# Optimization experiments

Hardware: AMD Instinct MI355X
Metric: run time of the kernel (lower is better)

Reference implementation:

```python
import jax, jax.numpy as jnp
import numpy as np

B, CIN, COUT, K, H, W = 16, 128, 256, 3, 56, 56
STRIDE = 1
PAD = K // 2


def setup_inputs() -> dict:
    key = jax.random.key(0)
    ks = jax.random.split(key, 12)
    x = jax.random.normal(ks[0], (B, CIN, H, W), dtype=jnp.float32)
    base_kernel = jax.random.normal(ks[1], (COUT, CIN, K, K), dtype=jnp.float32)
    bias = jnp.zeros((COUT,), dtype=jnp.float32)
    s = 1.0 / np.sqrt(CIN)
    fc_spatial_w = jax.random.uniform(ks[2], (K * K, CIN), minval=-s, maxval=s)
    fc_spatial_b = jax.random.uniform(ks[3], (K * K,), minval=-s, maxval=s)
    fc_in_w = jax.random.uniform(ks[4], (CIN, CIN), minval=-s, maxval=s)
    fc_in_b = jax.random.uniform(ks[5], (CIN,), minval=-s, maxval=s)
    fc_out_w = jax.random.uniform(ks[6], (COUT, CIN), minval=-s, maxval=s)
    fc_out_b = jax.random.uniform(ks[7], (COUT,), minval=-s, maxval=s)
    fc_kernel_w = jax.random.uniform(ks[8], (COUT * CIN * K * K, CIN), minval=-s, maxval=s)
    fc_kernel_b = jax.random.uniform(ks[9], (COUT * CIN * K * K,), minval=-s, maxval=s)
    return {
        "x": x, "base_kernel": base_kernel, "bias": bias,
        "fc_spatial_w": fc_spatial_w, "fc_spatial_b": fc_spatial_b,
        "fc_in_w": fc_in_w, "fc_in_b": fc_in_b,
        "fc_out_w": fc_out_w, "fc_out_b": fc_out_b,
        "fc_kernel_w": fc_kernel_w, "fc_kernel_b": fc_kernel_b,
    }


def _odconv(x, base_kernel, bias, fc_spatial_w, fc_spatial_b, fc_in_w, fc_in_b,
            fc_out_w, fc_out_b, fc_kernel_w, fc_kernel_b):
    b = x.shape[0]
    # global average pool -> context [B, Cin]
    context = jnp.mean(x, axis=(2, 3))
    sig = jax.nn.sigmoid
    attn_spatial = sig(context @ fc_spatial_w.T + fc_spatial_b).reshape(b, 1, 1, K, K)
    attn_in = sig(context @ fc_in_w.T + fc_in_b).reshape(b, 1, CIN, 1, 1)
    attn_out = sig(context @ fc_out_w.T + fc_out_b).reshape(b, COUT, 1, 1, 1)
    attn_kernel = sig(context @ fc_kernel_w.T + fc_kernel_b).reshape(b, COUT, CIN, K, K)
    # 5-way broadcast multiply -> per-sample dynamic kernel [B, Cout, Cin, K, K]
    dyn = base_kernel[None] * attn_out * attn_in * attn_spatial * attn_kernel

    def conv_one(xi, wi):
        # xi: [Cin, H, W], wi: [Cout, Cin, K, K]
        out = jax.lax.conv_general_dilated(
            xi[None], wi,
            window_strides=(STRIDE, STRIDE),
            padding=[(PAD, PAD), (PAD, PAD)],
            dimension_numbers=("NCHW", "OIHW", "NCHW"),
        )
        return out[0]

    out = jax.vmap(conv_one)(x, dyn)  # [B, Cout, H', W']
    return out + bias[None, :, None, None]


def reference(x, base_kernel, bias, fc_spatial_w, fc_spatial_b, fc_in_w, fc_in_b,
              fc_out_w, fc_out_b, fc_kernel_w, fc_kernel_b):
    return _odconv(x, base_kernel, bias, fc_spatial_w, fc_spatial_b, fc_in_w, fc_in_b,
                   fc_out_w, fc_out_b, fc_kernel_w, fc_kernel_b)
```

## Files before the change

kernel.cpp:

```cpp
#include <hip/hip_runtime.h>
#include <hip/hip_bf16.h>
#include <math.h>

#define BATCH 16
#define CIN   128
#define COUT  256
#define HH    56
#define WW    56
#define HW    3136
#define NTAP  9
#define NE    (COUT*CIN*NTAP)

typedef short short8 __attribute__((ext_vector_type(8)));
typedef float floatx4 __attribute__((ext_vector_type(4)));

#define WSB_CTX   0
#define WSB_ASP   8192
#define WSB_AIN   9472
#define WSB_AOUT  17664
#define WSB_ZP    34048
#define WSB_XT    38144
#define WSB_DYN   (WSB_XT + BATCH*HW*CIN*2)

static __device__ inline unsigned short f2b(float f) {
    union { float f; unsigned u; } v; v.f = f;
    unsigned r = v.u + 0x7FFF + ((v.u >> 16) & 1);
    return (unsigned short)(r >> 16);
}
static __device__ inline short8 pack8(float4 a, float4 b) {
    short8 r;
    r[0] = (short)f2b(a.x); r[1] = (short)f2b(a.y); r[2] = (short)f2b(a.z); r[3] = (short)f2b(a.w);
    r[4] = (short)f2b(b.x); r[5] = (short)f2b(b.y); r[6] = (short)f2b(b.z); r[7] = (short)f2b(b.w);
    return r;
}

typedef const __attribute__((address_space(1))) void* gas_ptr;
typedef __attribute__((address_space(3))) void* las_ptr;
static __device__ __forceinline__ void gl_lds16(const void* g, void* l) {
    __builtin_amdgcn_global_load_lds((gas_ptr)g, (las_ptr)l, 16, 0, 0);
}

__global__ void k_context(const float* __restrict__ x, float* __restrict__ ctx,
                          float* __restrict__ zp) {
    int bc = blockIdx.x;
    if (bc == 0 && threadIdx.x < 64) {
        uint4 z = {0u, 0u, 0u, 0u};
        ((uint4*)zp)[threadIdx.x] = z;
    }
    const float4* p = (const float4*)(x + (size_t)bc * HW);
    float s = 0.f;
    for (int i = threadIdx.x; i < HW / 4; i += 256) { float4 v = p[i]; s += v.x + v.y + v.z + v.w; }
    for (int off = 32; off; off >>= 1) s += __shfl_down(s, off, 64);
    __shared__ float red[4];
    if ((threadIdx.x & 63) == 0) red[threadIdx.x >> 6] = s;
    __syncthreads();
    if (threadIdx.x == 0) ctx[bc] = (red[0] + red[1] + red[2] + red[3]) * (1.f / (float)HW);
}

__global__ void k_attn(const float* __restrict__ ctx,
                       const float* __restrict__ wsp, const float* __restrict__ bsp,
                       const float* __restrict__ win, const float* __restrict__ bin,
                       const float* __restrict__ wout, const float* __restrict__ bout,
                       float* __restrict__ asp, float* __restrict__ ain, float* __restrict__ aout) {
    int R = blockIdx.x * 4 + (threadIdx.x >> 6);
    int lane = threadIdx.x & 63;
    int b = R / 393, r = R % 393;
    const float* w; float bias; float* o;
    if (r < 9)        { w = wsp  + r * CIN;         bias = bsp[r];         o = asp  + b * 16  + r; }
    else if (r < 137) { w = win  + (r - 9) * CIN;   bias = bin[r - 9];     o = ain  + b * CIN + (r - 9); }
    else              { w = wout + (r - 137) * CIN; bias = bout[r - 137];  o = aout + b * COUT + (r - 137); }
    float2 wv = ((const float2*)w)[lane];
    float2 cv = ((const float2*)(ctx + b * CIN))[lane];
    float d = wv.x * cv.x + wv.y * cv.y;
    for (int off = 32; off; off >>= 1) d += __shfl_down(d, off, 64);
    if (lane == 0) *o = 1.f / (1.f + __expf(-(d + bias)));
}

#define XT_BLOCKS    784
#define BUILD_BLOCKS 1152
__global__ void k_fat(const float* __restrict__ x, unsigned short* __restrict__ xt,
                      const float* __restrict__ ctx, const float* __restrict__ wk,
                      const float* __restrict__ bk, const float* __restrict__ base,
                      const float* __restrict__ asp, const float* __restrict__ ain,
                      const float* __restrict__ aout, unsigned short* __restrict__ dyn) {
    __shared__ unsigned short s_res[9 * 530 + 16];
    if (blockIdx.x < XT_BLOCKS) {
        int bid = blockIdx.x;
        int b = bid / 49;
        int p = (bid % 49) * 64 + (threadIdx.x & 63);
        int icq = threadIdx.x >> 6;
        const float* xb = x + (size_t)b * CIN * HW + p;
        unsigned short tmp[32];
#pragma unroll
        for (int j = 0; j < 32; ++j) tmp[j] = f2b(xb[(size_t)(icq * 32 + j) * HW]);
        uint4* dst = (uint4*)(xt + ((size_t)b * HW + p) * CIN + icq * 32);
        const uint4* s = (const uint4*)tmp;
        dst[0] = s[0]; dst[1] = s[1]; dst[2] = s[2]; dst[3] = s[3];
        return;
    }
    int bid = blockIdx.x - XT_BLOCKS;
    int wid = threadIdx.x >> 6, l = threadIdx.x & 63;
    int lq = l & 15, quad = l >> 4;
    int e0      = bid * 256;
    int siteMin = e0 / 9;

    short8 afr[4];
    const float* arow = ctx + lq * CIN;
#pragma unroll
    for (int kc = 0; kc < 4; ++kc) {
        float4 v0 = *(const float4*)(arow + kc * 32 + quad * 8);
        float4 v1 = *(const float4*)(arow + kc * 32 + quad * 8 + 4);
        afr[kc] = pack8(v0, v1);
    }

    int ebase = e0 + wid * 64;
    short8 bfr[4][4];
    float bke[4], bse[4];
#pragma unroll
    for (int j = 0; j < 4; ++j) {
        unsigned e = ebase + j * 16 + lq;
        const float* wrow = wk + (size_t)e * CIN;
#pragma unroll
        for (int kc = 0; kc < 4; ++kc) {
            float4 v0 = *(const float4*)(wrow + kc * 32 + quad * 8);
            float4 v1 = *(const float4*)(wrow + kc * 32 + quad * 8 + 4);
            bfr[j][kc] = pack8(v0, v1);
        }
        bke[j] = bk[e]; bse[j] = base[e];
    }
    floatx4 acc[4];
#pragma unroll
    for (int j = 0; j < 4; ++j) acc[j] = (floatx4){0.f, 0.f, 0.f, 0.f};
#pragma unroll
    for (int j = 0; j < 4; ++j)
#pragma unroll
        for (int kc = 0; kc < 4; ++kc)
            acc[j] = __builtin_amdgcn_mfma_f32_16x16x32_bf16(afr[kc], bfr[j][kc], acc[j], 0, 0, 0);
#pragma unroll
    for (int j = 0; j < 4; ++j) {
        unsigned e = ebase + j * 16 + lq;
        unsigned site = e / 9u, tap = e - site * 9u;
        unsigned oc = site >> 7, ic = site & 127;
        unsigned ds = site - siteMin;
#pragma unroll
        for (int r = 0; r < 4; ++r) {
            int b = quad * 4 + r;
            float s = 1.f / (1.f + __expf(-(acc[j][r] + bke[j])));
            float v = bse[j] * s * aout[b * COUT + oc] * ain[b * CIN + ic] * asp[b * 16 + tap];
            s_res[tap * 530 + b * 32 + ds] = f2b(v);
        }
    }
    __syncthreads();
    int hw_id = threadIdx.x >> 5;
    int hl    = threadIdx.x & 31;
#pragma unroll
    for (int it = 0; it < 18; ++it) {
        int pair = it * 8 + hw_id;
        int t = pair >> 4, b = pair & 15;
        int sLo = (e0 - t + 8) / 9;
        int sHi = (e0 + 255 - t) / 9;
        int cnt = sHi - sLo + 1;
        if (hl < cnt) {
            unsigned short v = s_res[t * 530 + b * 32 + (sLo - siteMin) + hl];
            dyn[(size_t)b * NE + t * 32768 + sLo + hl] = v;
        }
    }
}

__global__ __launch_bounds__(256, 2) void k_conv(
    const unsigned short* __restrict__ xt, const unsigned short* __restrict__ dyn,
    const float* __restrict__ bias, float* __restrict__ out,
    const unsigned short* __restrict__ zp) {
    __shared__ char s_x[640 * 64];
    __shared__ char s_a[576 * 64];
    int id  = blockIdx.x;
    int low = id & 7;
    int q   = id >> 3;
    int r   = q % 7;
    int phi = q / 7;
    int p   = phi * 8 + low;
    int oc0 = (p >> 4) * 64;
    int b   = p & 15;
    int r0  = r * 8;

    int tid = threadIdx.x;
    int wn = tid >> 6, l = tid & 63, lq = l & 15, quad = l >> 4;
    const unsigned short* xtb  = xt  + (size_t)b * HW * CIN;
    const unsigned short* dynb = dyn + (size_t)b * NE;

    int colx = wn * 16 + (l >> 2);
    int gxs  = colx - 1;
    bool gxok = (unsigned)gxs < (unsigned)WW;
    const unsigned short* zsrc = zp + l * 8;

    int pixaddr[7];
#pragma unroll
    for (int nf = 0; nf < 7; ++nf) {
        int n = nf * 16 + lq;
        int tr = wn * 2 + n / 56, col = n % 56;
        pixaddr[nf] = (tr * 64 + col) * 64 + quad * 16;
    }

    floatx4 acc[4][7];
#pragma unroll
    for (int i = 0; i < 4; ++i)
#pragma unroll
        for (int j = 0; j < 7; ++j) acc[i][j] = (floatx4){0.f, 0.f, 0.f, 0.f};

    for (int kc = 0; kc < 4; ++kc) {
        __syncthreads();
#pragma unroll
        for (int ry = 0; ry < 10; ++ry) {
            int gy = r0 + ry - 1;
            const unsigned short* src =
                (gxok && (unsigned)gy < (unsigned)HH)
                    ? xtb + (size_t)(gy * WW + gxs) * CIN + kc * 32 + (l & 3) * 8
                    : zsrc;
            gl_lds16(src, s_x + ry * 4096 + wn * 1024);
        }
#pragma unroll
        for (int i = 0; i < 9; ++i) {
            int u = i * 256 + tid;
            int icq2 = u & 3, oc = (u >> 2) & 63, tap = u >> 8;
            gl_lds16(dynb + (size_t)(tap * COUT + oc0 + oc) * CIN + kc * 32 + icq2 * 8,
                     s_a + i * 4096 + wn * 1024);
        }
        __syncthreads();
        __builtin_amdgcn_s_setprio(1);
#pragma unroll
        for (int tap = 0; tap < 9; ++tap) {
            short8 af[4];
#pragma unroll
            for (int mf = 0; mf < 4; ++mf)
                af[mf] = *(const short8*)(s_a + (tap * 64 + mf * 16 + lq) * 64 + quad * 16);
            int toff = (tap / 3) * 4096 + (tap % 3) * 64;
#pragma unroll
            for (int nf = 0; nf < 7; ++nf) {
                short8 bf = *(const short8*)(s_x + pixaddr[nf] + toff);
#pragma unroll
                for (int mf = 0; mf < 4; ++mf)
                    acc[mf][nf] = __builtin_amdgcn_mfma_f32_16x16x32_bf16(af[mf], bf, acc[mf][nf], 0, 0, 0);
            }
        }
        __builtin_amdgcn_s_setprio(0);
    }

#pragma unroll
    for (int mf = 0; mf < 4; ++mf) {
#pragma unroll
        for (int rr = 0; rr < 4; ++rr) {
            int oc = oc0 + mf * 16 + quad * 4 + rr;
            float bs = bias[oc];
            float* ob = out + (size_t)(b * COUT + oc) * HW + (r0 + wn * 2) * 56 + lq;
#pragma unroll
            for (int nf = 0; nf < 7; ++nf)
                ob[nf * 16] = acc[mf][nf][rr] + bs;
        }
    }
}

extern "C" void kernel_launch(void* const* d_in, const int* in_sizes, int n_in,
                              void* d_out, int out_size, void* d_ws, size_t ws_size,
                              hipStream_t stream) {
    const float* x    = (const float*)d_in[0];
    const float* base = (const float*)d_in[1];
    const float* bias = (const float*)d_in[2];
    const float* wsp  = (const float*)d_in[3];
    const float* bsp  = (const float*)d_in[4];
    const float* win  = (const float*)d_in[5];
    const float* bin  = (const float*)d_in[6];
    const float* wout = (const float*)d_in[7];
    const float* bout = (const float*)d_in[8];
    const float* wk   = (const float*)d_in[9];
    const float* bk   = (const float*)d_in[10];
    float* out = (float*)d_out;
    char* ws = (char*)d_ws;

    float* ctx  = (float*)(ws + WSB_CTX);
    float* asp  = (float*)(ws + WSB_ASP);
    float* ain  = (float*)(ws + WSB_AIN);
    float* aout = (float*)(ws + WSB_AOUT);
    float* zp   = (float*)(ws + WSB_ZP);
    unsigned short* xt  = (unsigned short*)(ws + WSB_XT);
    unsigned short* dyn = (unsigned short*)(ws + WSB_DYN);

    k_context<<<BATCH * CIN, 256, 0, stream>>>(x, ctx, zp);
    k_attn<<<(BATCH * 393) / 4, 256, 0, stream>>>(ctx, wsp, bsp, win, bin, wout, bout, asp, ain, aout);
    k_fat<<<XT_BLOCKS + BUILD_BLOCKS, 256, 0, stream>>>(x, xt, ctx, wk, bk, base, asp, ain, aout, dyn);
    k_conv<<<448, 256, 0, stream>>>(xt, dyn, bias, out, (const unsigned short*)zp);
}
```

Before: 313.9 us.

## Split fused transpose/build kernel; LDS-staged vectorized x transpose and register-pressure-reduced build

Splits the combined kernel into a dedicated x-transpose kernel and a dynamic-weight build kernel. The transpose now loads float4 along pixels into shared memory and writes 32-channel bf16 rows, replacing strided scalar loads. The build kernel processes its four column groups in two halves under launch_bounds(256,4) to cut register pressure and raise occupancy. It adds one kernel launch and loses any overlap between the transpose and build work inside a single grid.

```diff
diff --git a/kernel.cpp b/kernel.cpp
--- a/kernel.cpp
+++ b/kernel.cpp
@@ -76,29 +76,48 @@
     if (lane == 0) *o = 1.f / (1.f + __expf(-(d + bias)));
 }
 
-#define XT_BLOCKS    784
+#define XT_V2_BLOCKS (BATCH * 4 * 13)
+__global__ __launch_bounds__(256) void k_xt(const float* __restrict__ x,
+                                            unsigned short* __restrict__ xt) {
+    __shared__ unsigned short s[32 * 264];
+    int bid = blockIdx.x;
+    int b = bid / 52, rem = bid % 52;
+    int chg = rem / 13, ck = rem % 13;
+    int px0 = ck * 256;
+    int npx = HW - px0; if (npx > 256) npx = 256;
+    int tid = threadIdx.x;
+    const float* xb = x + ((size_t)(b * CIN + chg * 32)) * HW + px0;
+#pragma unroll
+    for (int pass = 0; pass < 8; ++pass) {
+        int i = pass * 256 + tid;
+        int c = i >> 6, p4 = i & 63;
+        int px = p4 * 4;
+        if (px < npx) {
+            float4 v = *(const float4*)(xb + (size_t)c * HW + px);
+            unsigned short h[4] = {f2b(v.x), f2b(v.y), f2b(v.z), f2b(v.w)};
+            *(uint2*)(&s[c * 264 + px]) = *(const uint2*)h;
+        }
+    }
+    __syncthreads();
+    int px = tid;
+    if (px < npx) {
+        unsigned short h[32];
+#pragma unroll
+        for (int c = 0; c < 32; ++c) h[c] = s[c * 264 + px];
+        uint4* dst = (uint4*)(xt + ((size_t)b * HW + px0 + px) * CIN + chg * 32);
+        const uint4* q = (const uint4*)h;
+        dst[0] = q[0]; dst[1] = q[1]; dst[2] = q[2]; dst[3] = q[3];
+    }
+}
+
 #define BUILD_BLOCKS 1152
-__global__ void k_fat(const float* __restrict__ x, unsigned short* __restrict__ xt,
-                      const float* __restrict__ ctx, const float* __restrict__ wk,
-                      const float* __restrict__ bk, const float* __restrict__ base,
-                      const float* __restrict__ asp, const float* __restrict__ ain,
-                      const float* __restrict__ aout, unsigned short* __restrict__ dyn) {
+__global__ __launch_bounds__(256, 4) void k_build(
+    const float* __restrict__ ctx, const float* __restrict__ wk,
+    const float* __restrict__ bk, const float* __restrict__ base,
+    const float* __restrict__ asp, const float* __restrict__ ain,
+    const float* __restrict__ aout, unsigned short* __restrict__ dyn) {
     __shared__ unsigned short s_res[9 * 530 + 16];
-    if (blockIdx.x < XT_BLOCKS) {
-        int bid = blockIdx.x;
-        int b = bid / 49;
-        int p = (bid % 49) * 64 + (threadIdx.x & 63);
-        int icq = threadIdx.x >> 6;
-        const float* xb = x + (size_t)b * CIN * HW + p;
-        unsigned short tmp[32];
-#pragma unroll
-        for (int j = 0; j < 32; ++j) tmp[j] = f2b(xb[(size_t)(icq * 32 + j) * HW]);
-        uint4* dst = (uint4*)(xt + ((size_t)b * HW + p) * CIN + icq * 32);
-        const uint4* s = (const uint4*)tmp;
-        dst[0] = s[0]; dst[1] = s[1]; dst[2] = s[2]; dst[3] = s[3];
-        return;
-    }
-    int bid = blockIdx.x - XT_BLOCKS;
+    int bid = blockIdx.x;
     int wid = threadIdx.x >> 6, l = threadIdx.x & 63;
     int lq = l & 15, quad = l >> 4;
     int e0      = bid * 256;
@@ -114,40 +133,44 @@
     }
 
     int ebase = e0 + wid * 64;
-    short8 bfr[4][4];
-    float bke[4], bse[4];
-#pragma unroll
-    for (int j = 0; j < 4; ++j) {
-        unsigned e = ebase + j * 16 + lq;
-        const float* wrow = wk + (size_t)e * CIN;
-#pragma unroll
-        for (int kc = 0; kc < 4; ++kc) {
-            float4 v0 = *(const float4*)(wrow + kc * 32 + quad * 8);
-            float4 v1 = *(const float4*)(wrow + kc * 32 + quad * 8 + 4);
-            bfr[j][kc] = pack8(v0, v1);
-        }
-        bke[j] = bk[e]; bse[j] = base[e];
-    }
-    floatx4 acc[4];
-#pragma unroll
-    for (int j = 0; j < 4; ++j) acc[j] = (floatx4){0.f, 0.f, 0.f, 0.f};
-#pragma unroll
-    for (int j = 0; j < 4; ++j)
-#pragma unroll
-        for (int kc = 0; kc < 4; ++kc)
-            acc[j] = __builtin_amdgcn_mfma_f32_16x16x32_bf16(afr[kc], bfr[j][kc], acc[j], 0, 0, 0);
-#pragma unroll
-    for (int j = 0; j < 4; ++j) {
-        unsigned e = ebase + j * 16 + lq;
-        unsigned site = e / 9u, tap = e - site * 9u;
-        unsigned oc = site >> 7, ic = site & 127;
-        unsigned ds = site - siteMin;
-#pragma unroll
-        for (int r = 0; r < 4; ++r) {
-            int b = quad * 4 + r;
-            float s = 1.f / (1.f + __expf(-(acc[j][r] + bke[j])));
-            float v = bse[j] * s * aout[b * COUT + oc] * ain[b * CIN + ic] * asp[b * 16 + tap];
-            s_res[tap * 530 + b * 32 + ds] = f2b(v);
+#pragma unroll
+    for (int jp = 0; jp < 2; ++jp) {
+        short8 bfr[2][4];
+        float bke[2], bse[2];
+        floatx4 acc[2];
+#pragma unroll
+        for (int u = 0; u < 2; ++u) {
+            int j = jp * 2 + u;
+            unsigned e = ebase + j * 16 + lq;
+            const float* wrow = wk + (size_t)e * CIN;
+#pragma unroll
+            for (int kc = 0; kc < 4; ++kc) {
+                float4 v0 = *(const float4*)(wrow + kc * 32 + quad * 8);
+                float4 v1 = *(const float4*)(wrow + kc * 32 + quad * 8 + 4);
+                bfr[u][kc] = pack8(v0, v1);
+            }
+            bke[u] = bk[e]; bse[u] = base[e];
+            acc[u] = (floatx4){0.f, 0.f, 0.f, 0.f};
+        }
+#pragma unroll
+        for (int u = 0; u < 2; ++u)
+#pragma unroll
+            for (int kc = 0; kc < 4; ++kc)
+                acc[u] = __builtin_amdgcn_mfma_f32_16x16x32_bf16(afr[kc], bfr[u][kc], acc[u], 0, 0, 0);
+#pragma unroll
+        for (int u = 0; u < 2; ++u) {
+            int j = jp * 2 + u;
+            unsigned e = ebase + j * 16 + lq;
+            unsigned site = e / 9u, tap = e - site * 9u;
+            unsigned oc = site >> 7, ic = site & 127;
+            unsigned ds = site - siteMin;
+#pragma unroll
+            for (int r = 0; r < 4; ++r) {
+                int bb = quad * 4 + r;
+                float sg = 1.f / (1.f + __expf(-(acc[u][r] + bke[u])));
+                float v = bse[u] * sg * aout[bb * COUT + oc] * ain[bb * CIN + ic] * asp[bb * 16 + tap];
+                s_res[tap * 530 + bb * 32 + ds] = f2b(v);
+            }
         }
     }
     __syncthreads();
@@ -286,6 +309,7 @@
 
     k_context<<<BATCH * CIN, 256, 0, stream>>>(x, ctx, zp);
     k_attn<<<(BATCH * 393) / 4, 256, 0, stream>>>(ctx, wsp, bsp, win, bin, wout, bout, asp, ain, aout);
-    k_fat<<<XT_BLOCKS + BUILD_BLOCKS, 256, 0, stream>>>(x, xt, ctx, wk, bk, base, asp, ain, aout, dyn);
+    k_xt<<<XT_V2_BLOCKS, 256, 0, stream>>>(x, xt);
+    k_build<<<BUILD_BLOCKS, 256, 0, stream>>>(ctx, wk, bk, base, asp, ain, aout, dyn);
     k_conv<<<448, 256, 0, stream>>>(xt, dyn, bias, out, (const unsigned short*)zp);
 }
```

New measurement: 313.5 us. About the same (-0.1%).
